# Performance work log

Hardware: AMD Instinct MI355X
Metric: run time of the kernel (lower is better)

## Reference

```python
import jax, jax.numpy as jnp
import numpy as np

N_NODES = 50000
N_EDGES = 800000
IN_DIM = 128
EDGE_DIM = 128
OUT_DIM = 128
N_AGG = 4          # mean, max, min, std
N_SCALE = 3        # identity, amplification, attenuation
AVG_D_LOG = float(np.log(17.0))  # log(avg_degree + 1), PNA avg_d['log']
EPS = 1e-5


def setup_inputs() -> dict:
    key = jax.random.key(0)
    ks = jax.random.split(key, 10)
    pre_in = 2 * IN_DIM + EDGE_DIM                      # pretrans input dim
    post_in = (N_AGG * N_SCALE + 1) * IN_DIM            # posttrans input dim
    return {
        "node_feat": jax.random.normal(ks[0], (N_NODES, IN_DIM), jnp.float32),
        "edge_feat": jax.random.normal(ks[1], (N_EDGES, EDGE_DIM), jnp.float32),
        "w_pre": jax.random.normal(ks[2], (pre_in, IN_DIM), jnp.float32) * (1.0 / np.sqrt(pre_in)),
        "b_pre": jnp.zeros((IN_DIM,), jnp.float32),
        "w_post1": jax.random.normal(ks[3], (post_in, OUT_DIM), jnp.float32) * (1.0 / np.sqrt(post_in)),
        "b_post1": jnp.zeros((OUT_DIM,), jnp.float32),
        "w_post2": jax.random.normal(ks[4], (OUT_DIM, OUT_DIM), jnp.float32) * (1.0 / np.sqrt(OUT_DIM)),
        "b_post2": jnp.zeros((OUT_DIM,), jnp.float32),
        "src": jax.random.randint(ks[5], (N_EDGES,), 0, N_NODES, jnp.int32),
        "dst": jax.random.randint(ks[6], (N_EDGES,), 0, N_NODES, jnp.int32),
    }


def reference(node_feat, edge_feat, w_pre, b_pre, w_post1, b_post1,
              w_post2, b_post2, src, dst):
    n = node_feat.shape[0]
    # --- pretrans over edges: MLP(cat[src_h, dst_h, edge_feat]) -> message ---
    z = jnp.concatenate([node_feat[src], node_feat[dst], edge_feat], axis=-1)  # [E, 2d+de]
    msg = jax.nn.relu(z @ w_pre + b_pre)                                       # [E, d]

    # --- multi-aggregator scatter-reduce per destination node ---
    ones = jnp.ones((msg.shape[0],), msg.dtype)
    deg = jax.ops.segment_sum(ones, dst, num_segments=n)                       # [N]
    d_safe = jnp.maximum(deg, 1.0)[:, None]
    has_nb = (deg > 0)[:, None]

    s1 = jax.ops.segment_sum(msg, dst, num_segments=n)
    s2 = jax.ops.segment_sum(msg * msg, dst, num_segments=n)
    a_mean = s1 / d_safe
    a_var = jax.nn.relu(s2 / d_safe - a_mean * a_mean)
    a_std = jnp.sqrt(a_var + EPS)
    a_max = jnp.where(has_nb, jax.ops.segment_max(msg, dst, num_segments=n), 0.0)
    a_min = jnp.where(has_nb, jax.ops.segment_min(msg, dst, num_segments=n), 0.0)
    agg = jnp.concatenate([a_mean, a_max, a_min, a_std], axis=-1)              # [N, 4d]

    # --- degree scalers: identity, amplification, attenuation ---
    logd = jnp.log(deg + 1.0)[:, None]
    amp = agg * (logd / AVG_D_LOG)
    att = agg * (AVG_D_LOG / jnp.maximum(logd, EPS))
    h = jnp.concatenate([node_feat, agg, amp, att], axis=-1)                   # [N, 13d]

    # --- posttrans MLP + residual ---
    h1 = jax.nn.relu(h @ w_post1 + b_post1)
    out = h1 @ w_post2 + b_post2 + node_feat                                   # residual (in_dim == out_dim)
    return out
```

## Files before the change

kernel.cpp:

```cpp
#include <hip/hip_runtime.h>
#include <math.h>

#define N_NODES 50000
#define N_EDGES 800000
#define D 128
#define AVG_D_LOG 2.833213344056216f
#define EPS 1e-5f

typedef __attribute__((ext_vector_type(8))) short bf16x8;
typedef __attribute__((ext_vector_type(4))) float f32x4;

__device__ __forceinline__ unsigned short f2bf(float x) {
    unsigned u = __float_as_uint(x);
    u += 0x7fffu + ((u >> 16) & 1u);
    return (unsigned short)(u >> 16);
}
__device__ __forceinline__ unsigned pk2bf(float a, float b) {
    return (unsigned)f2bf(a) | ((unsigned)f2bf(b) << 16);
}
__device__ __forceinline__ float bf2f(unsigned short u) {
    return __uint_as_float(((unsigned)u) << 16);
}

__global__ void k_init(int* hist, float* s1, float* s2, float* mx, float* mn) {
    size_t stride = (size_t)gridDim.x * blockDim.x;
    size_t i0 = (size_t)blockIdx.x * blockDim.x + threadIdx.x;
    const size_t ND4 = (size_t)N_NODES * D / 4;
    float4 z4 = {0.f, 0.f, 0.f, 0.f};
    int4 inf4 = {0x7f800000, 0x7f800000, 0x7f800000, 0x7f800000};
    for (size_t t = i0; t < ND4; t += stride) {
        ((float4*)s1)[t] = z4; ((float4*)s2)[t] = z4; ((float4*)mx)[t] = z4;
        ((int4*)mn)[t] = inf4;
    }
    for (size_t t = i0; t < N_NODES; t += stride) hist[t] = 0;
}

__global__ void k_prep(const float* __restrict__ wp, const float* __restrict__ w1,
                       const float* __restrict__ w2,
                       unsigned short* __restrict__ wpT, unsigned short* __restrict__ w1T,
                       unsigned short* __restrict__ w2T,
                       const int* __restrict__ dst, int* hist) {
    int b = blockIdx.x, t = threadIdx.x;
    if (b < 192) {
        int idx = b * 256 + t;
        int k = idx >> 7, c = idx & 127;
        wpT[(size_t)c * 384 + k] = f2bf(wp[idx]);
    } else if (b < 1024) {
        int idx = (b - 192) * 256 + t;
        int k = idx >> 7, c = idx & 127;
        w1T[(size_t)c * 1664 + k] = f2bf(w1[idx]);
    } else if (b < 1088) {
        int idx = (b - 1024) * 256 + t;
        int k = idx >> 7, c = idx & 127;
        w2T[(size_t)c * 128 + k] = f2bf(w2[idx]);
    } else {
        int e = (b - 1088) * 256 + t;
        if (e < N_EDGES) atomicAdd(&hist[dst[e]], 1);
    }
}

__global__ __launch_bounds__(1024) void k_scan(const int* __restrict__ hist, int* cursor) {
    __shared__ int part[1024];
    int t = threadIdx.x;
    const int chunk = (N_NODES + 1023) / 1024;
    int lo = t * chunk;
    int hi = lo + chunk; if (hi > N_NODES) hi = N_NODES;
    int s = 0;
    for (int i = lo; i < hi; ++i) s += hist[i];
    part[t] = s;
    __syncthreads();
    for (int off = 1; off < 1024; off <<= 1) {
        int v = (t >= off) ? part[t - off] : 0;
        __syncthreads();
        part[t] += v;
        __syncthreads();
    }
    int run = (t == 0) ? 0 : part[t - 1];
    for (int i = lo; i < hi; ++i) { cursor[i] = run; run += hist[i]; }
}

__global__ void k_scatter(const int* __restrict__ dst, int* cursor, int* perm) {
    int e = blockIdx.x * blockDim.x + threadIdx.x;
    if (e < N_EDGES) {
        int pos = atomicAdd(&cursor[dst[e]], 1);
        perm[pos] = e;
    }
}

#define MM256(ACC, AOFF, BOFF) do { \
    _Pragma("unroll") \
    for (int ks = 0; ks < 4; ++ks) { \
        bf16x8 afr[2], bfr[4]; \
        int kb = ks * 64 + lg * 16; \
        _Pragma("unroll") \
        for (int cf = 0; cf < 2; ++cf) { \
            int c = w * 32 + cf * 16 + lr; \
            afr[cf] = *(const bf16x8*)(smem + (AOFF) + c * 256 + (kb ^ ((c & 7) << 4))); \
        } \
        _Pragma("unroll") \
        for (int eb = 0; eb < 4; ++eb) { \
            int e = eb * 16 + lr; \
            bfr[eb] = *(const bf16x8*)(smem + (BOFF) + e * 256 + (kb ^ ((e & 7) << 4))); \
        } \
        _Pragma("unroll") \
        for (int cf = 0; cf < 2; ++cf) \
            _Pragma("unroll") \
            for (int eb = 0; eb < 4; ++eb) \
                ACC[cf][eb] = __builtin_amdgcn_mfma_f32_16x16x32_bf16( \
                    afr[cf], bfr[eb], ACC[cf][eb], 0, 0, 0); \
    } \
} while (0)

__global__ __launch_bounds__(256) void k_node(
    const float* __restrict__ nf, const unsigned short* __restrict__ wpT,
    const float* __restrict__ bp,
    unsigned short* __restrict__ p1, unsigned short* __restrict__ p2)
{
    __shared__ __align__(16) char smem[49152];
    __shared__ float sb[128];
    int t = threadIdx.x;
    int n0 = blockIdx.x * 64;
    if (t < 128) sb[t] = bp[t];
    int w = t >> 6, l = t & 63, lr = l & 15, lg = l >> 4;

    f32x4 acc1[2][4], acc2[2][4];
    #pragma unroll
    for (int i = 0; i < 2; ++i)
        #pragma unroll
        for (int j = 0; j < 4; ++j) { acc1[i][j] = (f32x4){0.f,0.f,0.f,0.f}; acc2[i][j] = (f32x4){0.f,0.f,0.f,0.f}; }

    #pragma unroll
    for (int p = 0; p < 8; ++p) {
        int g = t + 256 * p;
        int e = g >> 5, q = g & 31;
        int n = n0 + e;
        float4 fv = {0.f, 0.f, 0.f, 0.f};
        if (n < N_NODES) fv = *(const float4*)(nf + (size_t)n * D + q * 4);
        uint2 hv = { pk2bf(fv.x, fv.y), pk2bf(fv.z, fv.w) };
        *(uint2*)(smem + 32768 + e * 256 + ((q * 8) ^ ((e & 7) << 4))) = hv;
    }
    #pragma unroll
    for (int p = 0; p < 8; ++p) {
        int g = t + 256 * p;
        int c = g >> 4, j = g & 15;
        uint4 wv = *(const uint4*)(wpT + (size_t)c * 384 + j * 8);
        *(uint4*)(smem + c * 256 + ((j * 16) ^ ((c & 7) << 4))) = wv;
    }
    __syncthreads();
    MM256(acc1, 0, 32768);
    __syncthreads();
    #pragma unroll
    for (int p = 0; p < 8; ++p) {
        int g = t + 256 * p;
        int c = g >> 4, j = g & 15;
        uint4 wv = *(const uint4*)(wpT + (size_t)c * 384 + 128 + j * 8);
        *(uint4*)(smem + c * 256 + ((j * 16) ^ ((c & 7) << 4))) = wv;
    }
    __syncthreads();
    MM256(acc2, 0, 32768);
    __syncthreads();

    #pragma unroll
    for (int cf = 0; cf < 2; ++cf)
        #pragma unroll
        for (int eb = 0; eb < 4; ++eb) {
            int e  = eb * 16 + lr;
            int c0 = w * 32 + cf * 16 + lg * 4;
            uint2 v1 = { pk2bf(acc1[cf][eb][0], acc1[cf][eb][1]),
                         pk2bf(acc1[cf][eb][2], acc1[cf][eb][3]) };
            *(uint2*)(smem + e * 256 + ((c0 * 2) ^ ((e & 7) << 4))) = v1;
            uint2 v2 = { pk2bf(acc2[cf][eb][0] + sb[c0 + 0], acc2[cf][eb][1] + sb[c0 + 1]),
                         pk2bf(acc2[cf][eb][2] + sb[c0 + 2], acc2[cf][eb][3] + sb[c0 + 3]) };
            *(uint2*)(smem + 16384 + e * 256 + ((c0 * 2) ^ ((e & 7) << 4))) = v2;
        }
    __syncthreads();
    #pragma unroll
    for (int p = 0; p < 4; ++p) {
        int e = (t >> 4) + p * 16;
        int q = t & 15;
        int n = n0 + e;
        if (n < N_NODES) {
            int qq = q ^ (e & 7);
            uint4 v1 = *(const uint4*)(smem + e * 256 + q * 16);
            *(uint4*)(p1 + (size_t)n * D + qq * 8) = v1;
            uint4 v2 = *(const uint4*)(smem + 16384 + e * 256 + q * 16);
            *(uint4*)(p2 + (size_t)n * D + qq * 8) = v2;
        }
    }
}

__global__ __launch_bounds__(256) void k_edge(
    const float* __restrict__ ef, const unsigned short* __restrict__ wpT,
    const int* __restrict__ src, const int* __restrict__ dst,
    const unsigned short* __restrict__ p1, const unsigned short* __restrict__ p2,
    unsigned short* __restrict__ msgG)
{
    __shared__ __align__(16) char smem[49152];
    __shared__ int sidx[64], didx[64];

    int t = threadIdx.x;
    int e0 = blockIdx.x * 64;
    if (t < 64) { sidx[t] = src[e0 + t]; didx[t] = dst[e0 + t]; }
    int w = t >> 6, l = t & 63, lr = l & 15, lg = l >> 4;

    f32x4 acc[2][4];
    #pragma unroll
    for (int i = 0; i < 2; ++i)
        #pragma unroll
        for (int j = 0; j < 4; ++j) acc[i][j] = (f32x4){0.f, 0.f, 0.f, 0.f};

    #pragma unroll
    for (int p = 0; p < 8; ++p) {
        int g = t + 256 * p;
        int c = g >> 4, j = g & 15;
        uint4 wv = *(const uint4*)(wpT + (size_t)c * 384 + 256 + j * 8);
        *(uint4*)(smem + c * 256 + ((j * 16) ^ ((c & 7) << 4))) = wv;
    }
    #pragma unroll
    for (int p = 0; p < 8; ++p) {
        int g = t + 256 * p;
        int e = g >> 5, q = g & 31;
        float4 fv = *(const float4*)(ef + (size_t)(e0 + e) * D + q * 4);
        uint2 hv = { pk2bf(fv.x, fv.y), pk2bf(fv.z, fv.w) };
        *(uint2*)(smem + 32768 + e * 256 + ((q * 8) ^ ((e & 7) << 4))) = hv;
    }
    __syncthreads();
    MM256(acc, 0, 32768);
    __syncthreads();
    #pragma unroll
    for (int p = 0; p < 4; ++p) {
        int g = t + 256 * p;
        int e = g >> 4, q = g & 15;
        uint4 v1 = *(const uint4*)(p1 + (size_t)sidx[e] * D + q * 8);
        *(uint4*)(smem + e * 256 + ((q * 16) ^ ((e & 7) << 4))) = v1;
        uint4 v2 = *(const uint4*)(p2 + (size_t)didx[e] * D + q * 8);
        *(uint4*)(smem + 16384 + e * 256 + ((q * 16) ^ ((e & 7) << 4))) = v2;
    }
    __syncthreads();
    #pragma unroll
    for (int cf = 0; cf < 2; ++cf)
        #pragma unroll
        for (int eb = 0; eb < 4; ++eb) {
            int e  = eb * 16 + lr;
            int c0 = w * 32 + cf * 16 + lg * 4;
            uint2 a1 = *(const uint2*)(smem + e * 256 + ((c0 * 2) ^ ((e & 7) << 4)));
            uint2 a2 = *(const uint2*)(smem + 16384 + e * 256 + ((c0 * 2) ^ ((e & 7) << 4)));
            float v0 = acc[cf][eb][0] + bf2f((unsigned short)(a1.x & 0xffff)) + bf2f((unsigned short)(a2.x & 0xffff));
            float v1 = acc[cf][eb][1] + bf2f((unsigned short)(a1.x >> 16))    + bf2f((unsigned short)(a2.x >> 16));
            float v2 = acc[cf][eb][2] + bf2f((unsigned short)(a1.y & 0xffff)) + bf2f((unsigned short)(a2.y & 0xffff));
            float v3 = acc[cf][eb][3] + bf2f((unsigned short)(a1.y >> 16))    + bf2f((unsigned short)(a2.y >> 16));
            uint2 mv = { pk2bf(fmaxf(v0, 0.f), fmaxf(v1, 0.f)),
                         pk2bf(fmaxf(v2, 0.f), fmaxf(v3, 0.f)) };
            *(uint2*)(smem + 32768 + e * 256 + ((c0 * 2) ^ ((e & 7) << 4))) = mv;
        }
    __syncthreads();
    #pragma unroll
    for (int p = 0; p < 4; ++p) {
        int e = (t >> 4) + p * 16;
        int q = t & 15;
        uint4 v = *(const uint4*)(smem + 32768 + e * 256 + q * 16);
        int qq = q ^ (e & 7);
        *(uint4*)(msgG + (size_t)(e0 + e) * D + qq * 8) = v;
    }
}

__global__ __launch_bounds__(256) void k_agg(
    const unsigned short* __restrict__ msgG,
    const int* __restrict__ cursor, const int* __restrict__ hist,
    const int* __restrict__ perm,
    float* __restrict__ s1, float* __restrict__ s2,
    float* __restrict__ mx, float* __restrict__ mn, float* __restrict__ scal)
{
    int t = threadIdx.x;
    int n = blockIdx.x * 4 + (t >> 6);
    int tl = t & 63;
    int deg = hist[n];
    int re  = cursor[n];
    int rs  = re - deg;

    float sum0 = 0.f, sum1 = 0.f, sq0 = 0.f, sq1 = 0.f;
    float mx0 = -3.402823e38f, mx1 = -3.402823e38f;
    float mn0 =  3.402823e38f, mn1 =  3.402823e38f;
    const uint* mg = (const uint*)msgG;
    int pe_next = (deg > 0) ? perm[rs] : 0;
    for (int e = 0; e < deg; ++e) {
        int pe = pe_next;
        if (e + 1 < deg) pe_next = perm[rs + e + 1];
        uint v = mg[(size_t)pe * 64 + tl];
        float a = bf2f((unsigned short)(v & 0xffff));
        float b = bf2f((unsigned short)(v >> 16));
        sum0 += a; sum1 += b; sq0 += a * a; sq1 += b * b;
        mx0 = fmaxf(mx0, a); mx1 = fmaxf(mx1, b);
        mn0 = fminf(mn0, a); mn1 = fminf(mn1, b);
    }
    float dg = (float)deg;
    float ds = fmaxf(dg, 1.f);
    bool nb = deg > 0;
    float m0 = sum0 / ds, m1 = sum1 / ds;
    float sd0 = sqrtf(fmaxf(sq0 / ds - m0 * m0, 0.f) + EPS);
    float sd1 = sqrtf(fmaxf(sq1 / ds - m1 * m1, 0.f) + EPS);
    size_t base = (size_t)n * D + tl * 2;
    *(float2*)&s1[base] = (float2){m0, m1};
    *(float2*)&s2[base] = (float2){sd0, sd1};
    *(float2*)&mx[base] = (float2){nb ? mx0 : 0.f, nb ? mx1 : 0.f};
    *(float2*)&mn[base] = (float2){nb ? mn0 : 0.f, nb ? mn1 : 0.f};
    if (tl == 0) {
        float logd = logf(dg + 1.f);
        scal[2 * n]     = logd / AVG_D_LOG;
        scal[2 * n + 1] = AVG_D_LOG / fmaxf(logd, EPS);
    }
}

#define PFN(NC, PW0, PW1, PW2, PW3, PZ0, PZ1, PZ2, PZ3) do { \
    { int g = t;       int c = g >> 3, j = g & 7;  PW0 = *(const uint4*)(wpT + (size_t)c * 384 + (NC) * 64 + j * 8); } \
    { int g = t + 256; int c = g >> 3, j = g & 7;  PW1 = *(const uint4*)(wpT + (size_t)c * 384 + (NC) * 64 + j * 8); } \
    { int g = t + 512; int c = g >> 3, j = g & 7;  PW2 = *(const uint4*)(wpT + (size_t)c * 384 + (NC) * 64 + j * 8); } \
    { int g = t + 768; int c = g >> 3, j = g & 7;  PW3 = *(const uint4*)(wpT + (size_t)c * 384 + (NC) * 64 + j * 8); } \
    { int g = t;       int e = g >> 4, q = g & 15; PZ0 = *(const float4*)(ZROW(NC, e) + (((NC) & 1) * 64) + q * 4); } \
    { int g = t + 256; int e = g >> 4, q = g & 15; PZ1 = *(const float4*)(ZROW(NC, e) + (((NC) & 1) * 64) + q * 4); } \
    { int g = t + 512; int e = g >> 4, q = g & 15; PZ2 = *(const float4*)(ZROW(NC, e) + (((NC) & 1) * 64) + q * 4); } \
    { int g = t + 768; int e = g >> 4, q = g & 15; PZ3 = *(const float4*)(ZROW(NC, e) + (((NC) & 1) * 64) + q * 4); } \
} while (0)
#define WRN(OFF, PW0, PW1, PW2, PW3, PZ0, PZ1, PZ2, PZ3) do { \
    { int g = t;       int c = g >> 3, j = g & 7;  *(uint4*)(smem + (OFF) + c * 128 + ((j * 16) ^ ((c & 7) << 4))) = PW0; } \
    { int g = t + 256; int c = g >> 3, j = g & 7;  *(uint4*)(smem + (OFF) + c * 128 + ((j * 16) ^ ((c & 7) << 4))) = PW1; } \
    { int g = t + 512; int c = g >> 3, j = g & 7;  *(uint4*)(smem + (OFF) + c * 128 + ((j * 16) ^ ((c & 7) << 4))) = PW2; } \
    { int g = t + 768; int c = g >> 3, j = g & 7;  *(uint4*)(smem + (OFF) + c * 128 + ((j * 16) ^ ((c & 7) << 4))) = PW3; } \
    { int g = t;       int e = g >> 4, q = g & 15; uint2 hv = { pk2bf(PZ0.x, PZ0.y), pk2bf(PZ0.z, PZ0.w) }; \
      *(uint2*)(smem + (OFF) + 16384 + e * 128 + ((q * 8) ^ ((e & 7) << 4))) = hv; } \
    { int g = t + 256; int e = g >> 4, q = g & 15; uint2 hv = { pk2bf(PZ1.x, PZ1.y), pk2bf(PZ1.z, PZ1.w) }; \
      *(uint2*)(smem + (OFF) + 16384 + e * 128 + ((q * 8) ^ ((e & 7) << 4))) = hv; } \
    { int g = t + 512; int e = g >> 4, q = g & 15; uint2 hv = { pk2bf(PZ2.x, PZ2.y), pk2bf(PZ2.z, PZ2.w) }; \
      *(uint2*)(smem + (OFF) + 16384 + e * 128 + ((q * 8) ^ ((e & 7) << 4))) = hv; } \
    { int g = t + 768; int e = g >> 4, q = g & 15; uint2 hv = { pk2bf(PZ3.x, PZ3.y), pk2bf(PZ3.z, PZ3.w) }; \
      *(uint2*)(smem + (OFF) + 16384 + e * 128 + ((q * 8) ^ ((e & 7) << 4))) = hv; } \
} while (0)
#define MMO(OFF) do { \
    _Pragma("unroll") \
    for (int ks = 0; ks < 2; ++ks) { \
        bf16x8 afr[2], bfr[4]; \
        int kb = ks * 64 + lg * 16; \
        _Pragma("unroll") \
        for (int cf = 0; cf < 2; ++cf) { \
            int c = w * 32 + cf * 16 + lr; \
            afr[cf] = *(const bf16x8*)(smem + (OFF) + c * 128 + (kb ^ ((c & 7) << 4))); \
        } \
        _Pragma("unroll") \
        for (int eb = 0; eb < 4; ++eb) { \
            int e = eb * 16 + lr; \
            bfr[eb] = *(const bf16x8*)(smem + (OFF) + 16384 + e * 128 + (kb ^ ((e & 7) << 4))); \
        } \
        _Pragma("unroll") \
        for (int cf = 0; cf < 2; ++cf) \
            _Pragma("unroll") \
            for (int eb = 0; eb < 4; ++eb) \
                acc[cf][eb] = __builtin_amdgcn_mfma_f32_16x16x32_bf16( \
                    afr[cf], bfr[eb], acc[cf][eb], 0, 0, 0); \
    } \
} while (0)

__global__ __launch_bounds__(256) void k_pretrans(
    const float* __restrict__ nf, const float* __restrict__ ef,
    const unsigned short* __restrict__ wpT, const float* __restrict__ bp,
    const int* __restrict__ src, const int* __restrict__ dst,
    const int* __restrict__ perm,
    float* s1, float* s2, float* mx, float* mn)
{
    __shared__ __align__(16) char smem[24576];
    __shared__ int pidx[64], sidx[64], didx[64];
    __shared__ int seg_start[65], seg_dst[64];
    __shared__ int nseg_s;
    __shared__ float sb[128];

    int t = threadIdx.x;
    int e0 = blockIdx.x * 64;
    if (t < 64) {
        int pe = perm[e0 + t];
        pidx[t] = pe; sidx[t] = src[pe]; didx[t] = dst[pe];
    }
    if (t < 128) sb[t] = bp[t];
    __syncthreads();

    int w  = t >> 6;
    int l  = t & 63;
    int lr = l & 15;
    int lg = l >> 4;

    f32x4 acc[2][4];
    #pragma unroll
    for (int i = 0; i < 2; ++i)
        #pragma unroll
        for (int j = 0; j < 4; ++j) acc[i][j] = (f32x4){0.f, 0.f, 0.f, 0.f};

    uint4  pw0, pw1, pw2, pw3;
    float4 pz0, pz1, pz2, pz3;

#define ZROW(NC, e) ((NC) < 2 ? nf + (size_t)sidx[e] * D : \
                     (NC) < 4 ? nf + (size_t)didx[e] * D : \
                                ef + (size_t)pidx[e] * D)
    PFN(0, pw0, pw1, pw2, pw3, pz0, pz1, pz2, pz3);
    WRN(0, pw0, pw1, pw2, pw3, pz0, pz1, pz2, pz3); PFN(1, pw0, pw1, pw2, pw3, pz0, pz1, pz2, pz3); __syncthreads(); MMO(0); __syncthreads();
    WRN(0, pw0, pw1, pw2, pw3, pz0, pz1, pz2, pz3); PFN(2, pw0, pw1, pw2, pw3, pz0, pz1, pz2, pz3); __syncthreads(); MMO(0); __syncthreads();
    WRN(0, pw0, pw1, pw2, pw3, pz0, pz1, pz2, pz3); PFN(3, pw0, pw1, pw2, pw3, pz0, pz1, pz2, pz3); __syncthreads(); MMO(0); __syncthreads();
    WRN(0, pw0, pw1, pw2, pw3, pz0, pz1, pz2, pz3); PFN(4, pw0, pw1, pw2, pw3, pz0, pz1, pz2, pz3); __syncthreads(); MMO(0); __syncthreads();
    WRN(0, pw0, pw1, pw2, pw3, pz0, pz1, pz2, pz3); PFN(5, pw0, pw1, pw2, pw3, pz0, pz1, pz2, pz3); __syncthreads(); MMO(0); __syncthreads();
    WRN(0, pw0, pw1, pw2, pw3, pz0, pz1, pz2, pz3);                                                 __syncthreads(); MMO(0); __syncthreads();
#undef ZROW

    #pragma unroll
    for (int cf = 0; cf < 2; ++cf)
        #pragma unroll
        for (int eb = 0; eb < 4; ++eb) {
            int e  = eb * 16 + lr;
            int c0 = w * 32 + cf * 16 + lg * 4;
            float v0 = fmaxf(acc[cf][eb][0] + sb[c0 + 0], 0.f);
            float v1 = fmaxf(acc[cf][eb][1] + sb[c0 + 1], 0.f);
            float v2 = fmaxf(acc[cf][eb][2] + sb[c0 + 2], 0.f);
            float v3 = fmaxf(acc[cf][eb][3] + sb[c0 + 3], 0.f);
            uint2 mv = { pk2bf(v0, v1), pk2bf(v2, v3) };
            *(uint2*)(smem + e * 256 + ((c0 * 2) ^ ((e & 7) << 4))) = mv;
        }
    if (t == 0) {
        int ns = 0;
        for (int e = 0; e < 64; ++e) {
            if (e == 0 || didx[e] != didx[e - 1]) { seg_dst[ns] = didx[e]; seg_start[ns] = e; ++ns; }
        }
        seg_start[ns] = 64; nseg_s = ns;
    }
    __syncthreads();
    int nseg = nseg_s;
    for (int idx = t; idx < nseg * D; idx += 256) {
        int sg = idx >> 7, c = idx & 127;
        int eb2 = seg_start[sg], ee = seg_start[sg + 1];
        float s = 0.f, q = 0.f, vmax = 0.f, vmin = __int_as_float(0x7f800000);
        for (int e = eb2; e < ee; ++e) {
            float v = bf2f(*(const unsigned short*)(smem + e * 256 + ((c * 2) ^ ((e & 7) << 4))));
            s += v; q += v * v;
            vmax = fmaxf(vmax, v); vmin = fminf(vmin, v);
        }
        size_t base = (size_t)seg_dst[sg] * D + c;
        atomicAdd(&s1[base], s);
        atomicAdd(&s2[base], q);
        atomicMax((int*)&mx[base], __float_as_int(vmax));
        atomicMin((int*)&mn[base], __float_as_int(vmin));
    }
}

#undef PFN
#undef WRN
#undef MMO

__global__ void k_finalize(float* s1, float* s2, float* mx, float* mn,
                           const int* __restrict__ hist, float* scal) {
    size_t idx = (size_t)blockIdx.x * blockDim.x + threadIdx.x;
    if (idx >= (size_t)N_NODES * D) return;
    int n = (int)(idx >> 7);
    int c = (int)(idx & 127);
    float dg = (float)hist[n];
    float ds = fmaxf(dg, 1.f);
    float m  = s1[idx] / ds;
    float var = fmaxf(s2[idx] / ds - m * m, 0.f);
    float sd  = sqrtf(var + EPS);
    bool nb = dg > 0.f;
    s1[idx] = m;
    mx[idx] = nb ? mx[idx] : 0.f;
    mn[idx] = nb ? mn[idx] : 0.f;
    s2[idx] = sd;
    if (c == 0) {
        float logd = logf(dg + 1.f);
        scal[2 * n]     = logd / AVG_D_LOG;
        scal[2 * n + 1] = AVG_D_LOG / fmaxf(logd, EPS);
    }
}

__global__ __launch_bounds__(256, 3) void k_post(
    const float* __restrict__ nf,
    const float* __restrict__ amean, const float* __restrict__ amax,
    const float* __restrict__ amin,  const float* __restrict__ astd,
    const float* __restrict__ scal,
    const unsigned short* __restrict__ w1T, const float* __restrict__ b1,
    const unsigned short* __restrict__ w2T, const float* __restrict__ b2,
    float* __restrict__ out)
{
    __shared__ __align__(16) char smem[49152];
    __shared__ float samp[64], satt[64], sb1[128], sb2[128];

    int t = threadIdx.x;
    int n0 = blockIdx.x * 64;
    if (t < 64) {
        int n = n0 + t;
        samp[t] = (n < N_NODES) ? scal[2 * n] : 0.f;
        satt[t] = (n < N_NODES) ? scal[2 * n + 1] : 0.f;
    }
    if (t < 128) { sb1[t] = b1[t]; sb2[t] = b2[t]; }
    __syncthreads();

    int w  = t >> 6, l = t & 63, lr = l & 15, lg = l >> 4;
    f32x4 acc[2][4];
    #pragma unroll
    for (int i = 0; i < 2; ++i)
        #pragma unroll
        for (int j = 0; j < 4; ++j) acc[i][j] = (f32x4){0.f, 0.f, 0.f, 0.f};

    for (int chunk = 0; chunk < 13; ++chunk) {
        #pragma unroll
        for (int p = 0; p < 8; ++p) {
            int g = t + 256 * p;
            int c = g >> 4, j = g & 15;
            uint4 wv = *(const uint4*)(w1T + (size_t)c * 1664 + chunk * 128 + j * 8);
            *(uint4*)(smem + c * 256 + ((j * 16) ^ ((c & 7) << 4))) = wv;
        }
        const float* base;
        int r;
        if (chunk == 0) { base = nf; r = 0; }
        else {
            int b = (chunk - 1) & 3;
            r = (chunk - 1) >> 2;
            base = (b == 0) ? amean : (b == 1) ? amax : (b == 2) ? amin : astd;
        }
        #pragma unroll
        for (int p = 0; p < 8; ++p) {
            int g = t + 256 * p;
            int e = g >> 5, q = g & 31;
            int n = n0 + e;
            float4 fv = {0.f, 0.f, 0.f, 0.f};
            if (n < N_NODES) {
                fv = *(const float4*)(base + (size_t)n * D + q * 4);
                if (r == 1) { float sc = samp[e]; fv.x *= sc; fv.y *= sc; fv.z *= sc; fv.w *= sc; }
                else if (r == 2) { float sc = satt[e]; fv.x *= sc; fv.y *= sc; fv.z *= sc; fv.w *= sc; }
            }
            uint2 hv = { pk2bf(fv.x, fv.y), pk2bf(fv.z, fv.w) };
            *(uint2*)(smem + 32768 + e * 256 + ((q * 8) ^ ((e & 7) << 4))) = hv;
        }
        __syncthreads();
        MM256(acc, 0, 32768);
        __syncthreads();
    }

    #pragma unroll
    for (int cf = 0; cf < 2; ++cf)
        #pragma unroll
        for (int eb = 0; eb < 4; ++eb) {
            int e  = eb * 16 + lr;
            int c0 = w * 32 + cf * 16 + lg * 4;
            float v0 = fmaxf(acc[cf][eb][0] + sb1[c0 + 0], 0.f);
            float v1 = fmaxf(acc[cf][eb][1] + sb1[c0 + 1], 0.f);
            float v2 = fmaxf(acc[cf][eb][2] + sb1[c0 + 2], 0.f);
            float v3 = fmaxf(acc[cf][eb][3] + sb1[c0 + 3], 0.f);
            uint2 hv = { pk2bf(v0, v1), pk2bf(v2, v3) };
            *(uint2*)(smem + 32768 + e * 256 + ((c0 * 2) ^ ((e & 7) << 4))) = hv;
        }
    #pragma unroll
    for (int p = 0; p < 8; ++p) {
        int g = t + 256 * p;
        int c = g >> 4, j = g & 15;
        uint4 wv = *(const uint4*)(w2T + (size_t)c * 128 + j * 8);
        *(uint4*)(smem + c * 256 + ((j * 16) ^ ((c & 7) << 4))) = wv;
    }
    __syncthreads();

    f32x4 acc2[2][4];
    #pragma unroll
    for (int i = 0; i < 2; ++i)
        #pragma unroll
        for (int j = 0; j < 4; ++j) acc2[i][j] = (f32x4){0.f, 0.f, 0.f, 0.f};
    MM256(acc2, 0, 32768);

    #pragma unroll
    for (int cf = 0; cf < 2; ++cf)
        #pragma unroll
        for (int eb = 0; eb < 4; ++eb) {
            int n = n0 + eb * 16 + lr;
            if (n < N_NODES) {
                int c0 = w * 32 + cf * 16 + lg * 4;
                float4 rv = *(const float4*)(nf + (size_t)n * D + c0);
                float4 ov = { acc2[cf][eb][0] + sb2[c0 + 0] + rv.x,
                              acc2[cf][eb][1] + sb2[c0 + 1] + rv.y,
                              acc2[cf][eb][2] + sb2[c0 + 2] + rv.z,
                              acc2[cf][eb][3] + sb2[c0 + 3] + rv.w };
                *(float4*)(out + (size_t)n * D + c0) = ov;
            }
        }
}

extern "C" void kernel_launch(void* const* d_in, const int* in_sizes, int n_in,
                              void* d_out, int out_size, void* d_ws, size_t ws_size,
                              hipStream_t stream) {
    const float* nf = (const float*)d_in[0];
    const float* ef = (const float*)d_in[1];
    const float* wp = (const float*)d_in[2];
    const float* bp = (const float*)d_in[3];
    const float* w1 = (const float*)d_in[4];
    const float* b1 = (const float*)d_in[5];
    const float* w2 = (const float*)d_in[6];
    const float* b2 = (const float*)d_in[7];
    const int* src  = (const int*)d_in[8];
    const int* dst  = (const int*)d_in[9];
    float* out = (float*)d_out;

    const size_t ND = (size_t)N_NODES * D;
    const size_t MSG_SH = (size_t)N_EDGES * D;
    char* wsb = (char*)d_ws;
    int*   hist   = (int*)wsb;
    int*   cursor = hist + 50048;
    int*   perm   = cursor + 50048;
    unsigned short* wpT = (unsigned short*)(perm + N_EDGES);
    unsigned short* w1T = wpT + 49152;
    unsigned short* w2T = w1T + 212992;
    unsigned short* tail = w2T + 16384;

    unsigned short* p1   = tail;
    unsigned short* p2   = p1 + ND;
    unsigned short* msgG = p2 + ND;
    float* s1   = (float*)(msgG + MSG_SH);
    float* s2   = s1 + ND;
    float* mx   = s2 + ND;
    float* mn   = mx + ND;
    float* scal = mn + ND;
    size_t need_csr = (size_t)((char*)(scal + 100096) - wsb);

    bool use_csr = ws_size >= need_csr;
    if (!use_csr) {
        s1   = (float*)tail;
        s2   = s1 + ND;
        mx   = s2 + ND;
        mn   = mx + ND;
        scal = mn + ND;
    }

    if (use_csr) {
        hipMemsetAsync(hist, 0, N_NODES * sizeof(int), stream);
    } else {
        hipLaunchKernelGGL(k_init, dim3(2048), dim3(256), 0, stream, hist, s1, s2, mx, mn);
    }
    hipLaunchKernelGGL(k_prep, dim3(1088 + (N_EDGES + 255) / 256), dim3(256), 0, stream,
                       wp, w1, w2, wpT, w1T, w2T, dst, hist);
    hipLaunchKernelGGL(k_scan, dim3(1), dim3(1024), 0, stream, hist, cursor);
    hipLaunchKernelGGL(k_scatter, dim3((N_EDGES + 255) / 256), dim3(256), 0, stream, dst, cursor, perm);
    if (use_csr) {
        hipLaunchKernelGGL(k_node, dim3((N_NODES + 63) / 64), dim3(256), 0, stream,
                           nf, wpT, bp, p1, p2);
        hipLaunchKernelGGL(k_edge, dim3(N_EDGES / 64), dim3(256), 0, stream,
                           ef, wpT, src, dst, p1, p2, msgG);
        hipLaunchKernelGGL(k_agg, dim3(N_NODES / 4), dim3(256), 0, stream,
                           msgG, cursor, hist, perm, s1, s2, mx, mn, scal);
    } else {
        hipLaunchKernelGGL(k_pretrans, dim3(N_EDGES / 64), dim3(256), 0, stream,
                           nf, ef, wpT, bp, src, dst, perm, s1, s2, mx, mn);
        hipLaunchKernelGGL(k_finalize, dim3((unsigned)((ND + 255) / 256)), dim3(256), 0, stream,
                           s1, s2, mx, mn, hist, scal);
    }
    hipLaunchKernelGGL(k_post, dim3((N_NODES + 63) / 64), dim3(256), 0, stream,
                       nf, s1, mx, mn, s2, scal, w1T, b1, w2T, b2, out);
}
```

Before: 551.5 us.

## Store aggregates in bf16 and apply degree scalers post-GEMM in posttrans

Aggregation outputs (mean, max, min, std) are written as bf16 instead of fp32, halving their write and read traffic. The posttrans kernel loads each aggregate tile once and accumulates three separate GEMMs (identity, amp, att weight slices), then combines them with per-node scalers in the epilogue instead of re-reading and rescaling inputs three times. This adds accumulator registers, which may pressure occupancy, and changes where bf16 rounding happens relative to scaling.

```diff
diff --git a/kernel.cpp b/kernel.cpp
--- a/kernel.cpp
+++ b/kernel.cpp
@@ -268,8 +268,9 @@
     const unsigned short* __restrict__ msgG,
     const int* __restrict__ cursor, const int* __restrict__ hist,
     const int* __restrict__ perm,
-    float* __restrict__ s1, float* __restrict__ s2,
-    float* __restrict__ mx, float* __restrict__ mn, float* __restrict__ scal)
+    unsigned short* __restrict__ agm, unsigned short* __restrict__ ags,
+    unsigned short* __restrict__ agx, unsigned short* __restrict__ agn,
+    float* __restrict__ scal)
 {
     int t = threadIdx.x;
     int n = blockIdx.x * 4 + (t >> 6);
@@ -299,11 +300,11 @@
     float m0 = sum0 / ds, m1 = sum1 / ds;
     float sd0 = sqrtf(fmaxf(sq0 / ds - m0 * m0, 0.f) + EPS);
     float sd1 = sqrtf(fmaxf(sq1 / ds - m1 * m1, 0.f) + EPS);
-    size_t base = (size_t)n * D + tl * 2;
-    *(float2*)&s1[base] = (float2){m0, m1};
-    *(float2*)&s2[base] = (float2){sd0, sd1};
-    *(float2*)&mx[base] = (float2){nb ? mx0 : 0.f, nb ? mx1 : 0.f};
-    *(float2*)&mn[base] = (float2){nb ? mn0 : 0.f, nb ? mn1 : 0.f};
+    size_t ub = (size_t)n * 64 + tl;
+    ((uint*)agm)[ub] = pk2bf(m0, m1);
+    ((uint*)ags)[ub] = pk2bf(sd0, sd1);
+    ((uint*)agx)[ub] = pk2bf(nb ? mx0 : 0.f, nb ? mx1 : 0.f);
+    ((uint*)agn)[ub] = pk2bf(nb ? mn0 : 0.f, nb ? mn1 : 0.f);
     if (tl == 0) {
         float logd = logf(dg + 1.f);
         scal[2 * n]     = logd / AVG_D_LOG;
@@ -450,8 +451,10 @@
 #undef WRN
 #undef MMO
 
-__global__ void k_finalize(float* s1, float* s2, float* mx, float* mn,
-                           const int* __restrict__ hist, float* scal) {
+__global__ void k_finalize(const float* s1, const float* s2, const float* mx, const float* mn,
+                           const int* __restrict__ hist,
+                           unsigned short* agm, unsigned short* ags,
+                           unsigned short* agx, unsigned short* agn, float* scal) {
     size_t idx = (size_t)blockIdx.x * blockDim.x + threadIdx.x;
     if (idx >= (size_t)N_NODES * D) return;
     int n = (int)(idx >> 7);
@@ -462,10 +465,10 @@
     float var = fmaxf(s2[idx] / ds - m * m, 0.f);
     float sd  = sqrtf(var + EPS);
     bool nb = dg > 0.f;
-    s1[idx] = m;
-    mx[idx] = nb ? mx[idx] : 0.f;
-    mn[idx] = nb ? mn[idx] : 0.f;
-    s2[idx] = sd;
+    agm[idx] = f2bf(m);
+    agx[idx] = f2bf(nb ? mx[idx] : 0.f);
+    agn[idx] = f2bf(nb ? mn[idx] : 0.f);
+    ags[idx] = f2bf(sd);
     if (c == 0) {
         float logd = logf(dg + 1.f);
         scal[2 * n]     = logd / AVG_D_LOG;
@@ -475,8 +478,8 @@
 
 __global__ __launch_bounds__(256, 3) void k_post(
     const float* __restrict__ nf,
-    const float* __restrict__ amean, const float* __restrict__ amax,
-    const float* __restrict__ amin,  const float* __restrict__ astd,
+    const unsigned short* __restrict__ agm, const unsigned short* __restrict__ agx,
+    const unsigned short* __restrict__ agn, const unsigned short* __restrict__ ags,
     const float* __restrict__ scal,
     const unsigned short* __restrict__ w1T, const float* __restrict__ b1,
     const unsigned short* __restrict__ w2T, const float* __restrict__ b2,
@@ -496,57 +499,70 @@
     __syncthreads();
 
     int w  = t >> 6, l = t & 63, lr = l & 15, lg = l >> 4;
-    f32x4 acc[2][4];
+
+#define STW(CH) do { \
+    _Pragma("unroll") \
+    for (int p = 0; p < 8; ++p) { \
+        int g = t + 256 * p; \
+        int c = g >> 4, j = g & 15; \
+        uint4 wv = *(const uint4*)(w1T + (size_t)c * 1664 + (CH) * 128 + j * 8); \
+        *(uint4*)(smem + c * 256 + ((j * 16) ^ ((c & 7) << 4))) = wv; \
+    } \
+} while (0)
+
+    f32x4 accI[2][4], accA[2][4], accT[2][4];
     #pragma unroll
     for (int i = 0; i < 2; ++i)
         #pragma unroll
-        for (int j = 0; j < 4; ++j) acc[i][j] = (f32x4){0.f, 0.f, 0.f, 0.f};
-
-    for (int chunk = 0; chunk < 13; ++chunk) {
-        #pragma unroll
-        for (int p = 0; p < 8; ++p) {
+        for (int j = 0; j < 4; ++j) {
+            accI[i][j] = (f32x4){0.f,0.f,0.f,0.f};
+            accA[i][j] = (f32x4){0.f,0.f,0.f,0.f};
+            accT[i][j] = (f32x4){0.f,0.f,0.f,0.f};
+        }
+
+    #pragma unroll
+    for (int p = 0; p < 8; ++p) {
+        int g = t + 256 * p;
+        int e = g >> 5, q = g & 31;
+        int n = n0 + e;
+        float4 fv = {0.f, 0.f, 0.f, 0.f};
+        if (n < N_NODES) fv = *(const float4*)(nf + (size_t)n * D + q * 4);
+        uint2 hv = { pk2bf(fv.x, fv.y), pk2bf(fv.z, fv.w) };
+        *(uint2*)(smem + 32768 + e * 256 + ((q * 8) ^ ((e & 7) << 4))) = hv;
+    }
+    STW(0);
+    __syncthreads();
+    MM256(accI, 0, 32768);
+    __syncthreads();
+
+    for (int b = 0; b < 4; ++b) {
+        const unsigned short* ab = (b == 0) ? agm : (b == 1) ? agx : (b == 2) ? agn : ags;
+        #pragma unroll
+        for (int p = 0; p < 4; ++p) {
             int g = t + 256 * p;
-            int c = g >> 4, j = g & 15;
-            uint4 wv = *(const uint4*)(w1T + (size_t)c * 1664 + chunk * 128 + j * 8);
-            *(uint4*)(smem + c * 256 + ((j * 16) ^ ((c & 7) << 4))) = wv;
-        }
-        const float* base;
-        int r;
-        if (chunk == 0) { base = nf; r = 0; }
-        else {
-            int b = (chunk - 1) & 3;
-            r = (chunk - 1) >> 2;
-            base = (b == 0) ? amean : (b == 1) ? amax : (b == 2) ? amin : astd;
-        }
-        #pragma unroll
-        for (int p = 0; p < 8; ++p) {
-            int g = t + 256 * p;
-            int e = g >> 5, q = g & 31;
+            int e = g >> 4, q = g & 15;
             int n = n0 + e;
-            float4 fv = {0.f, 0.f, 0.f, 0.f};
-            if (n < N_NODES) {
-                fv = *(const float4*)(base + (size_t)n * D + q * 4);
-                if (r == 1) { float sc = samp[e]; fv.x *= sc; fv.y *= sc; fv.z *= sc; fv.w *= sc; }
-                else if (r == 2) { float sc = satt[e]; fv.x *= sc; fv.y *= sc; fv.z *= sc; fv.w *= sc; }
-            }
-            uint2 hv = { pk2bf(fv.x, fv.y), pk2bf(fv.z, fv.w) };
-            *(uint2*)(smem + 32768 + e * 256 + ((q * 8) ^ ((e & 7) << 4))) = hv;
-        }
-        __syncthreads();
-        MM256(acc, 0, 32768);
-        __syncthreads();
-    }
+            uint4 v = {0u, 0u, 0u, 0u};
+            if (n < N_NODES) v = *(const uint4*)(ab + (size_t)n * D + q * 8);
+            *(uint4*)(smem + 32768 + e * 256 + ((q * 16) ^ ((e & 7) << 4))) = v;
+        }
+        STW(1 + b); __syncthreads(); MM256(accI, 0, 32768); __syncthreads();
+        STW(5 + b); __syncthreads(); MM256(accA, 0, 32768); __syncthreads();
+        STW(9 + b); __syncthreads(); MM256(accT, 0, 32768); __syncthreads();
+    }
+#undef STW
 
     #pragma unroll
     for (int cf = 0; cf < 2; ++cf)
         #pragma unroll
         for (int eb = 0; eb < 4; ++eb) {
             int e  = eb * 16 + lr;
+            float sa = samp[e], st = satt[e];
             int c0 = w * 32 + cf * 16 + lg * 4;
-            float v0 = fmaxf(acc[cf][eb][0] + sb1[c0 + 0], 0.f);
-            float v1 = fmaxf(acc[cf][eb][1] + sb1[c0 + 1], 0.f);
-            float v2 = fmaxf(acc[cf][eb][2] + sb1[c0 + 2], 0.f);
-            float v3 = fmaxf(acc[cf][eb][3] + sb1[c0 + 3], 0.f);
+            float v0 = fmaxf(accI[cf][eb][0] + sa * accA[cf][eb][0] + st * accT[cf][eb][0] + sb1[c0 + 0], 0.f);
+            float v1 = fmaxf(accI[cf][eb][1] + sa * accA[cf][eb][1] + st * accT[cf][eb][1] + sb1[c0 + 1], 0.f);
+            float v2 = fmaxf(accI[cf][eb][2] + sa * accA[cf][eb][2] + st * accT[cf][eb][2] + sb1[c0 + 2], 0.f);
+            float v3 = fmaxf(accI[cf][eb][3] + sa * accA[cf][eb][3] + st * accT[cf][eb][3] + sb1[c0 + 3], 0.f);
             uint2 hv = { pk2bf(v0, v1), pk2bf(v2, v3) };
             *(uint2*)(smem + 32768 + e * 256 + ((c0 * 2) ^ ((e & 7) << 4))) = hv;
         }
@@ -612,20 +628,25 @@
     unsigned short* p1   = tail;
     unsigned short* p2   = p1 + ND;
     unsigned short* msgG = p2 + ND;
-    float* s1   = (float*)(msgG + MSG_SH);
-    float* s2   = s1 + ND;
-    float* mx   = s2 + ND;
-    float* mn   = mx + ND;
-    float* scal = mn + ND;
+    unsigned short* agm  = msgG + MSG_SH;
+    unsigned short* agx  = agm + ND;
+    unsigned short* agn  = agx + ND;
+    unsigned short* ags  = agn + ND;
+    float* scal          = (float*)(ags + ND);
     size_t need_csr = (size_t)((char*)(scal + 100096) - wsb);
 
+    float *s1 = nullptr, *s2 = nullptr, *mx = nullptr, *mn = nullptr;
     bool use_csr = ws_size >= need_csr;
     if (!use_csr) {
         s1   = (float*)tail;
         s2   = s1 + ND;
         mx   = s2 + ND;
         mn   = mx + ND;
-        scal = mn + ND;
+        agm  = (unsigned short*)(mn + ND);
+        agx  = agm + ND;
+        agn  = agx + ND;
+        ags  = agn + ND;
+        scal = (float*)(ags + ND);
     }
 
     if (use_csr) {
@@ -643,13 +664,13 @@
         hipLaunchKernelGGL(k_edge, dim3(N_EDGES / 64), dim3(256), 0, stream,
                            ef, wpT, src, dst, p1, p2, msgG);
         hipLaunchKernelGGL(k_agg, dim3(N_NODES / 4), dim3(256), 0, stream,
-                           msgG, cursor, hist, perm, s1, s2, mx, mn, scal);
+                           msgG, cursor, hist, perm, agm, ags, agx, agn, scal);
     } else {
         hipLaunchKernelGGL(k_pretrans, dim3(N_EDGES / 64), dim3(256), 0, stream,
                            nf, ef, wpT, bp, src, dst, perm, s1, s2, mx, mn);
         hipLaunchKernelGGL(k_finalize, dim3((unsigned)((ND + 255) / 256)), dim3(256), 0, stream,
-                           s1, s2, mx, mn, hist, scal);
+                           s1, s2, mx, mn, hist, agm, ags, agx, agn, scal);
     }
     hipLaunchKernelGGL(k_post, dim3((N_NODES + 63) / 64), dim3(256), 0, stream,
-                       nf, s1, mx, mn, s2, scal, w1T, b1, w2T, b2, out);
-}
+                       nf, agm, agx, agn, ags, scal, w1T, b1, w2T, b2, out);
+}
```

New measurement: 561.6 us. About the same (+1.8%).

## Pipeline edge GEMM K-chunks via registers, gather node projections directly, shuffle perm indices

Applied to the files above, without the earlier changes.

The edge kernel now splits the edge-feature GEMM into two 64-wide K chunks. The second chunk's weights and features are prefetched into registers while the first is multiplied, which halves LDS use to 24KB and should raise occupancy. The src/dst projection gathers no longer stage through shared memory; each lane reads its values straight from global memory in the epilogue, removing a sync and an LDS round trip but issuing smaller uncoalesced 8-byte loads. The aggregation kernel loads up to 64 perm indices in one coalesced load per wave and broadcasts them with shuffles instead of reading them serially.

```diff
diff --git a/kernel.cpp b/kernel.cpp
--- a/kernel.cpp
+++ b/kernel.cpp
@@ -195,7 +195,7 @@
     const unsigned short* __restrict__ p1, const unsigned short* __restrict__ p2,
     unsigned short* __restrict__ msgG)
 {
-    __shared__ __align__(16) char smem[49152];
+    __shared__ __align__(16) char smem[24576];
     __shared__ int sidx[64], didx[64];
 
     int t = threadIdx.x;
@@ -209,56 +209,86 @@
         #pragma unroll
         for (int j = 0; j < 4; ++j) acc[i][j] = (f32x4){0.f, 0.f, 0.f, 0.f};
 
-    #pragma unroll
-    for (int p = 0; p < 8; ++p) {
-        int g = t + 256 * p;
-        int c = g >> 4, j = g & 15;
-        uint4 wv = *(const uint4*)(wpT + (size_t)c * 384 + 256 + j * 8);
-        *(uint4*)(smem + c * 256 + ((j * 16) ^ ((c & 7) << 4))) = wv;
-    }
-    #pragma unroll
-    for (int p = 0; p < 8; ++p) {
-        int g = t + 256 * p;
-        int e = g >> 5, q = g & 31;
-        float4 fv = *(const float4*)(ef + (size_t)(e0 + e) * D + q * 4);
-        uint2 hv = { pk2bf(fv.x, fv.y), pk2bf(fv.z, fv.w) };
-        *(uint2*)(smem + 32768 + e * 256 + ((q * 8) ^ ((e & 7) << 4))) = hv;
-    }
-    __syncthreads();
-    MM256(acc, 0, 32768);
-    __syncthreads();
-    #pragma unroll
-    for (int p = 0; p < 4; ++p) {
-        int g = t + 256 * p;
-        int e = g >> 4, q = g & 15;
-        uint4 v1 = *(const uint4*)(p1 + (size_t)sidx[e] * D + q * 8);
-        *(uint4*)(smem + e * 256 + ((q * 16) ^ ((e & 7) << 4))) = v1;
-        uint4 v2 = *(const uint4*)(p2 + (size_t)didx[e] * D + q * 8);
-        *(uint4*)(smem + 16384 + e * 256 + ((q * 16) ^ ((e & 7) << 4))) = v2;
-    }
-    __syncthreads();
+    uint4  pw0, pw1, pw2, pw3;
+    float4 pz0, pz1, pz2, pz3;
+
+#define EPF(CH) do { \
+    { int g = t;       int c = g >> 3, j = g & 7;  pw0 = *(const uint4*)(wpT + (size_t)c * 384 + 256 + (CH) * 64 + j * 8); } \
+    { int g = t + 256; int c = g >> 3, j = g & 7;  pw1 = *(const uint4*)(wpT + (size_t)c * 384 + 256 + (CH) * 64 + j * 8); } \
+    { int g = t + 512; int c = g >> 3, j = g & 7;  pw2 = *(const uint4*)(wpT + (size_t)c * 384 + 256 + (CH) * 64 + j * 8); } \
+    { int g = t + 768; int c = g >> 3, j = g & 7;  pw3 = *(const uint4*)(wpT + (size_t)c * 384 + 256 + (CH) * 64 + j * 8); } \
+    { int g = t;       int e = g >> 4, q = g & 15; pz0 = *(const float4*)(ef + (size_t)(e0 + e) * D + (CH) * 64 + q * 4); } \
+    { int g = t + 256; int e = g >> 4, q = g & 15; pz1 = *(const float4*)(ef + (size_t)(e0 + e) * D + (CH) * 64 + q * 4); } \
+    { int g = t + 512; int e = g >> 4, q = g & 15; pz2 = *(const float4*)(ef + (size_t)(e0 + e) * D + (CH) * 64 + q * 4); } \
+    { int g = t + 768; int e = g >> 4, q = g & 15; pz3 = *(const float4*)(ef + (size_t)(e0 + e) * D + (CH) * 64 + q * 4); } \
+} while (0)
+#define EWR() do { \
+    { int g = t;       int c = g >> 3, j = g & 7;  *(uint4*)(smem + c * 128 + ((j * 16) ^ ((c & 7) << 4))) = pw0; } \
+    { int g = t + 256; int c = g >> 3, j = g & 7;  *(uint4*)(smem + c * 128 + ((j * 16) ^ ((c & 7) << 4))) = pw1; } \
+    { int g = t + 512; int c = g >> 3, j = g & 7;  *(uint4*)(smem + c * 128 + ((j * 16) ^ ((c & 7) << 4))) = pw2; } \
+    { int g = t + 768; int c = g >> 3, j = g & 7;  *(uint4*)(smem + c * 128 + ((j * 16) ^ ((c & 7) << 4))) = pw3; } \
+    { int g = t;       int e = g >> 4, q = g & 15; uint2 hv = { pk2bf(pz0.x, pz0.y), pk2bf(pz0.z, pz0.w) }; \
+      *(uint2*)(smem + 16384 + e * 128 + ((q * 8) ^ ((e & 7) << 4))) = hv; } \
+    { int g = t + 256; int e = g >> 4, q = g & 15; uint2 hv = { pk2bf(pz1.x, pz1.y), pk2bf(pz1.z, pz1.w) }; \
+      *(uint2*)(smem + 16384 + e * 128 + ((q * 8) ^ ((e & 7) << 4))) = hv; } \
+    { int g = t + 512; int e = g >> 4, q = g & 15; uint2 hv = { pk2bf(pz2.x, pz2.y), pk2bf(pz2.z, pz2.w) }; \
+      *(uint2*)(smem + 16384 + e * 128 + ((q * 8) ^ ((e & 7) << 4))) = hv; } \
+    { int g = t + 768; int e = g >> 4, q = g & 15; uint2 hv = { pk2bf(pz3.x, pz3.y), pk2bf(pz3.z, pz3.w) }; \
+      *(uint2*)(smem + 16384 + e * 128 + ((q * 8) ^ ((e & 7) << 4))) = hv; } \
+} while (0)
+#define EMM() do { \
+    _Pragma("unroll") \
+    for (int ks = 0; ks < 2; ++ks) { \
+        bf16x8 afr[2], bfr[4]; \
+        int kb = ks * 64 + lg * 16; \
+        _Pragma("unroll") \
+        for (int cf = 0; cf < 2; ++cf) { \
+            int c = w * 32 + cf * 16 + lr; \
+            afr[cf] = *(const bf16x8*)(smem + c * 128 + (kb ^ ((c & 7) << 4))); \
+        } \
+        _Pragma("unroll") \
+        for (int eb = 0; eb < 4; ++eb) { \
+            int e = eb * 16 + lr; \
+            bfr[eb] = *(const bf16x8*)(smem + 16384 + e * 128 + (kb ^ ((e & 7) << 4))); \
+        } \
+        _Pragma("unroll") \
+        for (int cf = 0; cf < 2; ++cf) \
+            _Pragma("unroll") \
+            for (int eb = 0; eb < 4; ++eb) \
+                acc[cf][eb] = __builtin_amdgcn_mfma_f32_16x16x32_bf16( \
+                    afr[cf], bfr[eb], acc[cf][eb], 0, 0, 0); \
+    } \
+} while (0)
+
+    EPF(0);
+    EWR(); EPF(1); __syncthreads(); EMM(); __syncthreads();
+    EWR();         __syncthreads(); EMM(); __syncthreads();
+#undef EPF
+#undef EWR
+#undef EMM
+
     #pragma unroll
     for (int cf = 0; cf < 2; ++cf)
         #pragma unroll
         for (int eb = 0; eb < 4; ++eb) {
             int e  = eb * 16 + lr;
             int c0 = w * 32 + cf * 16 + lg * 4;
-            uint2 a1 = *(const uint2*)(smem + e * 256 + ((c0 * 2) ^ ((e & 7) << 4)));
-            uint2 a2 = *(const uint2*)(smem + 16384 + e * 256 + ((c0 * 2) ^ ((e & 7) << 4)));
+            uint2 a1 = *(const uint2*)(p1 + (size_t)sidx[e] * D + c0);
+            uint2 a2 = *(const uint2*)(p2 + (size_t)didx[e] * D + c0);
             float v0 = acc[cf][eb][0] + bf2f((unsigned short)(a1.x & 0xffff)) + bf2f((unsigned short)(a2.x & 0xffff));
             float v1 = acc[cf][eb][1] + bf2f((unsigned short)(a1.x >> 16))    + bf2f((unsigned short)(a2.x >> 16));
             float v2 = acc[cf][eb][2] + bf2f((unsigned short)(a1.y & 0xffff)) + bf2f((unsigned short)(a2.y & 0xffff));
             float v3 = acc[cf][eb][3] + bf2f((unsigned short)(a1.y >> 16))    + bf2f((unsigned short)(a2.y >> 16));
             uint2 mv = { pk2bf(fmaxf(v0, 0.f), fmaxf(v1, 0.f)),
                          pk2bf(fmaxf(v2, 0.f), fmaxf(v3, 0.f)) };
-            *(uint2*)(smem + 32768 + e * 256 + ((c0 * 2) ^ ((e & 7) << 4))) = mv;
+            *(uint2*)(smem + e * 256 + ((c0 * 2) ^ ((e & 7) << 4))) = mv;
         }
     __syncthreads();
     #pragma unroll
     for (int p = 0; p < 4; ++p) {
         int e = (t >> 4) + p * 16;
         int q = t & 15;
-        uint4 v = *(const uint4*)(smem + 32768 + e * 256 + q * 16);
+        uint4 v = *(const uint4*)(smem + e * 256 + q * 16);
         int qq = q ^ (e & 7);
         *(uint4*)(msgG + (size_t)(e0 + e) * D + qq * 8) = v;
     }
@@ -282,10 +312,20 @@
     float mx0 = -3.402823e38f, mx1 = -3.402823e38f;
     float mn0 =  3.402823e38f, mn1 =  3.402823e38f;
     const uint* mg = (const uint*)msgG;
-    int pe_next = (deg > 0) ? perm[rs] : 0;
-    for (int e = 0; e < deg; ++e) {
-        int pe = pe_next;
-        if (e + 1 < deg) pe_next = perm[rs + e + 1];
+
+    int pe_lane = (tl < deg) ? perm[rs + tl] : 0;
+    int dmin = (deg < 64) ? deg : 64;
+    for (int e = 0; e < dmin; ++e) {
+        int pe = __shfl(pe_lane, e);
+        uint v = mg[(size_t)pe * 64 + tl];
+        float a = bf2f((unsigned short)(v & 0xffff));
+        float b = bf2f((unsigned short)(v >> 16));
+        sum0 += a; sum1 += b; sq0 += a * a; sq1 += b * b;
+        mx0 = fmaxf(mx0, a); mx1 = fmaxf(mx1, b);
+        mn0 = fminf(mn0, a); mn1 = fminf(mn1, b);
+    }
+    for (int e = 64; e < deg; ++e) {
+        int pe = perm[rs + e];
         uint v = mg[(size_t)pe * 64 + tl];
         float a = bf2f((unsigned short)(v & 0xffff));
         float b = bf2f((unsigned short)(v >> 16));
```

Measured after the change: 586.4 us. 1.06x slower.
